# Performance work log

Measured on AMD Instinct MI355X. Metric: run time of the kernel, lower is better.

## Reference

```python
import jax, jax.numpy as jnp
import numpy as np

B, S, D, H = 4, 2048, 1024, 16
HD = D // H


def setup_inputs() -> dict:
    key = jax.random.key(0)
    k1, k2, k3 = jax.random.split(key, 3)
    x = jax.random.normal(k1, (B, S, D), dtype=jnp.float32)
    # xavier-ish scaling for stable softmax
    W_attn = jax.random.normal(k2, (3 * D, D), dtype=jnp.float32) * (1.0 / np.sqrt(2 * D))
    b_attn = jnp.zeros((3 * D,), dtype=jnp.float32)
    W_out = jax.random.normal(k3, (D, D), dtype=jnp.float32) * (1.0 / np.sqrt(D))
    b_out = jnp.zeros((D,), dtype=jnp.float32)
    return {"x": x, "W_attn": W_attn, "b_attn": b_attn, "W_out": W_out, "b_out": b_out}


def reference(x, W_attn, b_attn, W_out, b_out):
    bs, seq, d = x.shape
    # fused QKV projection (torch Linear: y = x @ W.T + b)
    kqv = jnp.einsum("bsd,ed->bse", x, W_attn) + b_attn
    # NOTE: source splits as k, q, v (k first)
    k, q, v = jnp.split(kqv, 3, axis=2)
    # [b, s, h, hd] -> [b, h, s, hd]
    k = k.reshape(bs, seq, H, HD).transpose(0, 2, 1, 3)
    q = q.reshape(bs, seq, H, HD).transpose(0, 2, 1, 3)
    v = v.reshape(bs, seq, H, HD).transpose(0, 2, 1, 3)
    scale = 1.0 / np.sqrt(HD)
    scores = jnp.einsum("bhqd,bhkd->bhqk", q, k) * scale
    attn = jax.nn.softmax(scores, axis=-1)
    y = jnp.einsum("bhqk,bhkd->bhqd", attn, v)
    y = y.transpose(0, 2, 1, 3).reshape(bs, seq, d)
    out = jnp.einsum("bsd,ed->bse", y, W_out) + b_out
    return out
```

## Files before the change

### kernel.cpp

```cpp
#include <hip/hip_runtime.h>

typedef unsigned short u16;
typedef unsigned int u32;
typedef __attribute__((ext_vector_type(2))) u32 u32x2;
typedef __attribute__((ext_vector_type(4))) u32 u32x4;
typedef __attribute__((ext_vector_type(8))) short bf16x8;
typedef __attribute__((ext_vector_type(4))) float f32x4;

__device__ __forceinline__ u16 f2bf(float f) {
  u32 b = __float_as_uint(f);
  b += 0x7fffu + ((b >> 16) & 1u);
  return (u16)(b >> 16);
}

__device__ __forceinline__ u32 pk2bf(float a, float b) {
#if __has_builtin(__builtin_amdgcn_cvt_pk_bf16_f32)
  return __builtin_bit_cast(u32, __builtin_amdgcn_cvt_pk_bf16_f32(a, b));
#else
  return (u32)f2bf(a) | ((u32)f2bf(b) << 16);
#endif
}

__device__ __forceinline__ float fexp2(float x) {
#if __has_builtin(__builtin_amdgcn_exp2f)
  return __builtin_amdgcn_exp2f(x);
#else
  return exp2f(x);
#endif
}

__device__ __forceinline__ void gload_lds16(const u16* g, u16* l) {
  __builtin_amdgcn_global_load_lds((const __attribute__((address_space(1))) void*)g,
                                   (__attribute__((address_space(3))) void*)l, 16, 0, 0);
}

__global__ __launch_bounds__(256) void cvt_f32_bf16(const float* __restrict__ in,
                                                    u16* __restrict__ out) {
  long i = ((long)blockIdx.x * 256 + threadIdx.x) * 8;
  u32 u[8];
#pragma unroll
  for (int j = 0; j < 8; j++) {
    u32 b = __float_as_uint(in[i + j]);
    u[j] = (b + 0x7fffu + ((b >> 16) & 1u)) >> 16;
  }
  u32x4 o;
  o[0] = u[0] | (u[1] << 16);
  o[1] = u[2] | (u[3] << 16);
  o[2] = u[4] | (u[5] << 16);
  o[3] = u[6] | (u[7] << 16);
  *(u32x4*)(out + i) = o;
}

__device__ __forceinline__ void gemm_core_128(const u16* __restrict__ A,
                                              const u16* __restrict__ B, int K,
                                              int m0, int n0, u16* As, u16* Bs,
                                              f32x4 acc[4][4]) {
  int t = threadIdx.x;
  int lane = t & 63, w = t >> 6;
  int quad = lane >> 4, l16 = lane & 15;
  int wm = (w >> 1) * 64, wn = (w & 1) * 64;
  int lr = lane >> 3, lc = lane & 7;
  int cg = lc ^ lr;
  int swz = l16 & 7;
  for (int k0 = 0; k0 < K; k0 += 64) {
#pragma unroll
    for (int i = 0; i < 4; i++) {
      int r0 = i * 32 + w * 8;
      gload_lds16(&A[(long)(m0 + r0 + lr) * K + k0 + cg * 8], &As[r0 * 64]);
      gload_lds16(&B[(long)(n0 + r0 + lr) * K + k0 + cg * 8], &Bs[r0 * 64]);
    }
    __syncthreads();
#pragma unroll
    for (int ks = 0; ks < 2; ks++) {
      bf16x8 a[4], b[4];
#pragma unroll
      for (int tm = 0; tm < 4; tm++)
        a[tm] = *(const bf16x8*)&As[(wm + tm * 16 + l16) * 64 + ((ks * 4 + quad) ^ swz) * 8];
#pragma unroll
      for (int tn = 0; tn < 4; tn++)
        b[tn] = *(const bf16x8*)&Bs[(wn + tn * 16 + l16) * 64 + ((ks * 4 + quad) ^ swz) * 8];
#pragma unroll
      for (int tm = 0; tm < 4; tm++)
#pragma unroll
        for (int tn = 0; tn < 4; tn++)
          acc[tm][tn] = __builtin_amdgcn_mfma_f32_16x16x32_bf16(a[tm], b[tn],
                                                                acc[tm][tn], 0, 0, 0);
    }
    __syncthreads();
  }
}

#define QSCALE 0.1803368801f
__global__ __launch_bounds__(256) void gemm_qkv(const u16* __restrict__ A,
                                                const u16* __restrict__ B,
                                                const float* __restrict__ bias,
                                                u16* __restrict__ Kg,
                                                u16* __restrict__ Qg,
                                                u16* __restrict__ Vg) {
  __shared__ __align__(16) u16 As[128 * 64];
  __shared__ __align__(16) u16 Bs[128 * 64];
  const int K = 1024;
  int m0 = blockIdx.y * 128, n0 = blockIdx.x * 128;
  f32x4 acc[4][4];
#pragma unroll
  for (int i = 0; i < 4; i++)
#pragma unroll
    for (int j = 0; j < 4; j++) acc[i][j] = (f32x4)0.0f;
  gemm_core_128(A, B, K, m0, n0, As, Bs, acc);

  int t = threadIdx.x, lane = t & 63, w = t >> 6;
  int quad = lane >> 4, l16 = lane & 15;
  int wm = (w >> 1) * 64, wn = (w & 1) * 64;
#pragma unroll
  for (int tn = 0; tn < 4; tn++) {
    int n = n0 + wn + tn * 16 + l16;
    float bv = bias[n];
    int which = n >> 10;
    int h = (n >> 6) & 15, d = n & 63;
#pragma unroll
    for (int tm = 0; tm < 4; tm++) {
      int m = m0 + wm + tm * 16 + quad * 4;
      int b = m >> 11, s = m & 2047;
      long bh = (long)b * 16 + h;
      if (which == 2) {
        u32x2 pk;
        pk[0] = pk2bf(acc[tm][tn][0] + bv, acc[tm][tn][1] + bv);
        pk[1] = pk2bf(acc[tm][tn][2] + bv, acc[tm][tn][3] + bv);
        *(u32x2*)&Vg[(bh * 64 + d) * 2048 + s] = pk;
      } else {
#pragma unroll
        for (int r = 0; r < 4; r++) {
          float v = acc[tm][tn][r] + bv;
          if (which == 0)
            Kg[(bh * 2048 + s + r) * 64 + d] = f2bf(v);
          else
            Qg[(bh * 2048 + s + r) * 64 + d] = f2bf(v * QSCALE);
        }
      }
    }
  }
}

__global__ __launch_bounds__(256) void gemm_out(const u16* __restrict__ A,
                                                const u16* __restrict__ B,
                                                const float* __restrict__ bias,
                                                float* __restrict__ out) {
  __shared__ __align__(16) u16 As[128 * 64];
  __shared__ __align__(16) u16 Bs[128 * 64];
  const int K = 1024, N = 1024;
  int m0 = blockIdx.y * 128, n0 = blockIdx.x * 128;
  f32x4 acc[4][4];
#pragma unroll
  for (int i = 0; i < 4; i++)
#pragma unroll
    for (int j = 0; j < 4; j++) acc[i][j] = (f32x4)0.0f;
  gemm_core_128(A, B, K, m0, n0, As, Bs, acc);

  int t = threadIdx.x, lane = t & 63, w = t >> 6;
  int quad = lane >> 4, l16 = lane & 15;
  int wm = (w >> 1) * 64, wn = (w & 1) * 64;
#pragma unroll
  for (int tn = 0; tn < 4; tn++) {
    int n = n0 + wn + tn * 16 + l16;
    float bv = bias[n];
#pragma unroll
    for (int tm = 0; tm < 4; tm++) {
#pragma unroll
      for (int r = 0; r < 4; r++) {
        int m = m0 + wm + tm * 16 + quad * 4 + r;
        out[(long)m * N + n] = acc[tm][tn][r] + bv;
      }
    }
  }
}

__global__ __launch_bounds__(256, 4) void attn_kernel(const u16* __restrict__ Qg,
                                                      const u16* __restrict__ Kg,
                                                      const u16* __restrict__ Vg,
                                                      u16* __restrict__ Y) {
  __shared__ __align__(16) u16 Ks[64 * 64];
  __shared__ __align__(16) u16 Vs[64 * 64];
  __shared__ __align__(16) u16 Ps[4 * 32 * 64];
  int t = threadIdx.x, lane = t & 63, w = t >> 6;
  int quad = lane >> 4, l16 = lane & 15;
  int bh = blockIdx.y;
  int q0 = blockIdx.x * 128 + w * 32;
  u16* Pw = Ps + w * 32 * 64;
  int lr = lane >> 3, lc = lane & 7, cg = lc ^ lr;
  int swz = l16 & 7;

  bf16x8 qf[2][2];
#pragma unroll
  for (int tq = 0; tq < 2; tq++) {
    const u16* qp = Qg + ((long)bh * 2048 + q0 + tq * 16 + l16) * 64;
    qf[tq][0] = *(const bf16x8*)(qp + quad * 8);
    qf[tq][1] = *(const bf16x8*)(qp + 32 + quad * 8);
  }

  float lsum[2] = {0.0f, 0.0f};
  f32x4 acc[4][2];
#pragma unroll
  for (int tn = 0; tn < 4; tn++)
#pragma unroll
    for (int tq = 0; tq < 2; tq++) acc[tn][tq] = (f32x4)0.0f;

  for (int kv0 = 0; kv0 < 2048; kv0 += 64) {
#pragma unroll
    for (int j = 0; j < 2; j++) {
      int r0 = j * 32 + w * 8;
      gload_lds16(&Kg[((long)bh * 2048 + kv0 + r0 + lr) * 64 + cg * 8], &Ks[r0 * 64]);
      gload_lds16(&Vg[((long)bh * 64 + r0 + lr) * 2048 + kv0 + cg * 8], &Vs[r0 * 64]);
    }
    __syncthreads();

    bf16x8 kf[4][2];
#pragma unroll
    for (int tn = 0; tn < 4; tn++)
#pragma unroll
      for (int ks = 0; ks < 2; ks++)
        kf[tn][ks] = *(const bf16x8*)&Ks[(tn * 16 + l16) * 64 + ((ks * 4 + quad) ^ swz) * 8];

#pragma unroll
    for (int tq = 0; tq < 2; tq++) {
      f32x4 s[4];
#pragma unroll
      for (int tn = 0; tn < 4; tn++) s[tn] = (f32x4)0.0f;
#pragma unroll
      for (int ks = 0; ks < 2; ks++)
#pragma unroll
        for (int tn = 0; tn < 4; tn++)
          s[tn] = __builtin_amdgcn_mfma_f32_16x16x32_bf16(kf[tn][ks], qf[tq][ks],
                                                          s[tn], 0, 0, 0);
      int qrow = tq * 16 + l16;
#pragma unroll
      for (int tn = 0; tn < 4; tn++) {
        float e0 = fexp2(s[tn][0]);
        float e1 = fexp2(s[tn][1]);
        float e2 = fexp2(s[tn][2]);
        float e3 = fexp2(s[tn][3]);
        lsum[tq] += (e0 + e1) + (e2 + e3);
        u32x2 pk;
        pk[0] = pk2bf(e0, e1);
        pk[1] = pk2bf(e2, e3);
        int c2 = ((tn * 2 + (quad >> 1)) ^ swz) * 2 + (quad & 1);
        *(u32x2*)&Pw[qrow * 64 + c2 * 4] = pk;
      }
    }

#pragma unroll
    for (int ks = 0; ks < 2; ks++) {
      bf16x8 vf[4];
#pragma unroll
      for (int tn = 0; tn < 4; tn++)
        vf[tn] = *(const bf16x8*)&Vs[(tn * 16 + l16) * 64 + ((ks * 4 + quad) ^ swz) * 8];
#pragma unroll
      for (int tq = 0; tq < 2; tq++) {
        bf16x8 pf = *(const bf16x8*)&Pw[(tq * 16 + l16) * 64 + ((ks * 4 + quad) ^ swz) * 8];
#pragma unroll
        for (int tn = 0; tn < 4; tn++)
          acc[tn][tq] = __builtin_amdgcn_mfma_f32_16x16x32_bf16(vf[tn], pf,
                                                                acc[tn][tq], 0, 0, 0);
      }
    }
    __syncthreads();
  }

#pragma unroll
  for (int tq = 0; tq < 2; tq++) {
    lsum[tq] += __shfl_xor(lsum[tq], 16, 64);
    lsum[tq] += __shfl_xor(lsum[tq], 32, 64);
  }

  int b = bh >> 4, h = bh & 15;
#pragma unroll
  for (int tq = 0; tq < 2; tq++) {
    float inv = 1.0f / lsum[tq];
    long row = (long)b * 2048 + q0 + tq * 16 + l16;
#pragma unroll
    for (int tn = 0; tn < 4; tn++) {
      u32x2 pk;
      pk[0] = pk2bf(acc[tn][tq][0] * inv, acc[tn][tq][1] * inv);
      pk[1] = pk2bf(acc[tn][tq][2] * inv, acc[tn][tq][3] * inv);
      *(u32x2*)&Y[row * 1024 + h * 64 + tn * 16 + quad * 4] = pk;
    }
  }
}

extern "C" void kernel_launch(void* const* d_in, const int* in_sizes, int n_in,
                              void* d_out, int out_size, void* d_ws, size_t ws_size,
                              hipStream_t stream) {
  const float* x = (const float*)d_in[0];
  const float* W_attn = (const float*)d_in[1];
  const float* b_attn = (const float*)d_in[2];
  const float* W_out = (const float*)d_in[3];
  const float* b_out = (const float*)d_in[4];
  float* out = (float*)d_out;

  char* ws = (char*)d_ws;
  u16* xb = (u16*)ws;
  u16* Wab = (u16*)(ws + 16777216);
  u16* Wob = (u16*)(ws + 16777216 + 6291456);
  u16* Kg = (u16*)(ws + 25165824);
  u16* Qg = Kg + 8388608;
  u16* Vg = Qg + 8388608;
  u16* Yb = xb;

  cvt_f32_bf16<<<4096, 256, 0, stream>>>(x, xb);
  cvt_f32_bf16<<<1536, 256, 0, stream>>>(W_attn, Wab);
  cvt_f32_bf16<<<512, 256, 0, stream>>>(W_out, Wob);

  gemm_qkv<<<dim3(24, 64), 256, 0, stream>>>(xb, Wab, b_attn, Kg, Qg, Vg);
  attn_kernel<<<dim3(16, 64), 256, 0, stream>>>(Qg, Kg, Vg, Yb);
  gemm_out<<<dim3(8, 64), 256, 0, stream>>>(Yb, Wob, b_out, out);
}
```

Measured before the change: 292.2 us.

## Double-buffer K/V tiles and keep P in registers for PV MFMA

The attention kernel now double-buffers the K and V LDS tiles, so the next tile's global-to-LDS load is issued while the current tile is being computed. The probability tile no longer round-trips through shared memory. The exponentiated scores stay in registers and feed 16x16x16 bf16 MFMAs directly, with V fragments read in the matching layout. This removes the P store/load traffic and one barrier's worth of LDS usage. The cost is twice as many PV MFMA instructions, each with half the K depth, and the double-buffered prefetch has only one barrier per iteration, which could risk an LDS race.

Result: no change. 291.6 us (-0.2%).

```diff
diff --git a/kernel.cpp b/kernel.cpp
--- a/kernel.cpp
+++ b/kernel.cpp
@@ -5,6 +5,7 @@
 typedef __attribute__((ext_vector_type(2))) u32 u32x2;
 typedef __attribute__((ext_vector_type(4))) u32 u32x4;
 typedef __attribute__((ext_vector_type(8))) short bf16x8;
+typedef __attribute__((ext_vector_type(4))) short bf16x4;
 typedef __attribute__((ext_vector_type(4))) float f32x4;
 
 __device__ __forceinline__ u16 f2bf(float f) {
@@ -21,11 +22,31 @@
 #endif
 }
 
+__device__ __forceinline__ bf16x4 mk_bf16x4(u32 lo, u32 hi) {
+  u32x2 t;
+  t[0] = lo;
+  t[1] = hi;
+  return __builtin_bit_cast(bf16x4, t);
+}
+
 __device__ __forceinline__ float fexp2(float x) {
 #if __has_builtin(__builtin_amdgcn_exp2f)
   return __builtin_amdgcn_exp2f(x);
 #else
   return exp2f(x);
+#endif
+}
+
+__device__ __forceinline__ f32x4 mfma16x16x16(bf16x4 a, bf16x4 b, f32x4 c) {
+#if __has_builtin(__builtin_amdgcn_mfma_f32_16x16x16bf16_1k)
+  return __builtin_amdgcn_mfma_f32_16x16x16bf16_1k(a, b, c, 0, 0, 0);
+#elif __has_builtin(__builtin_amdgcn_mfma_f32_16x16x16_bf16)
+  return __builtin_amdgcn_mfma_f32_16x16x16_bf16(a, b, c, 0, 0, 0);
+#else
+  asm volatile("v_mfma_f32_16x16x16_bf16 %0, %1, %2, %0\n\ts_nop 7\n\ts_nop 7"
+               : "+v"(c)
+               : "v"(a), "v"(b));
+  return c;
 #endif
 }
 
@@ -178,14 +199,12 @@
                                                       const u16* __restrict__ Kg,
                                                       const u16* __restrict__ Vg,
                                                       u16* __restrict__ Y) {
-  __shared__ __align__(16) u16 Ks[64 * 64];
-  __shared__ __align__(16) u16 Vs[64 * 64];
-  __shared__ __align__(16) u16 Ps[4 * 32 * 64];
+  __shared__ __align__(16) u16 Ks[2][64 * 64];
+  __shared__ __align__(16) u16 Vs[2][64 * 64];
   int t = threadIdx.x, lane = t & 63, w = t >> 6;
   int quad = lane >> 4, l16 = lane & 15;
   int bh = blockIdx.y;
   int q0 = blockIdx.x * 128 + w * 32;
-  u16* Pw = Ps + w * 32 * 64;
   int lr = lane >> 3, lc = lane & 7, cg = lc ^ lr;
   int swz = l16 & 7;
 
@@ -200,26 +219,43 @@
   float lsum[2] = {0.0f, 0.0f};
   f32x4 acc[4][2];
 #pragma unroll
-  for (int tn = 0; tn < 4; tn++)
-#pragma unroll
-    for (int tq = 0; tq < 2; tq++) acc[tn][tq] = (f32x4)0.0f;
-
-  for (int kv0 = 0; kv0 < 2048; kv0 += 64) {
-#pragma unroll
-    for (int j = 0; j < 2; j++) {
-      int r0 = j * 32 + w * 8;
-      gload_lds16(&Kg[((long)bh * 2048 + kv0 + r0 + lr) * 64 + cg * 8], &Ks[r0 * 64]);
-      gload_lds16(&Vg[((long)bh * 64 + r0 + lr) * 2048 + kv0 + cg * 8], &Vs[r0 * 64]);
-    }
-    __syncthreads();
+  for (int dt = 0; dt < 4; dt++)
+#pragma unroll
+    for (int tq = 0; tq < 2; tq++) acc[dt][tq] = (f32x4)0.0f;
+
+  const u16* Kbase = Kg + ((long)bh * 2048 + lr) * 64 + cg * 8;
+  const u16* Vbase = Vg + ((long)bh * 64 + lr) * 2048 + cg * 8;
+
+#pragma unroll
+  for (int j = 0; j < 2; j++) {
+    int r0 = j * 32 + w * 8;
+    gload_lds16(Kbase + (long)r0 * 64, &Ks[0][r0 * 64]);
+    gload_lds16(Vbase + (long)r0 * 2048, &Vs[0][r0 * 64]);
+  }
+  __syncthreads();
+
+  int cur = 0;
+  for (int kv0 = 0; kv0 < 2048; kv0 += 64, cur ^= 1) {
+    if (kv0 + 64 < 2048) {
+      int kn = kv0 + 64;
+#pragma unroll
+      for (int j = 0; j < 2; j++) {
+        int r0 = j * 32 + w * 8;
+        gload_lds16(Kbase + (long)(kn + r0) * 64, &Ks[cur ^ 1][r0 * 64]);
+        gload_lds16(Vbase + (long)r0 * 2048 + kn, &Vs[cur ^ 1][r0 * 64]);
+      }
+    }
+    const u16* Kc = Ks[cur];
+    const u16* Vc = Vs[cur];
 
     bf16x8 kf[4][2];
 #pragma unroll
     for (int tn = 0; tn < 4; tn++)
 #pragma unroll
       for (int ks = 0; ks < 2; ks++)
-        kf[tn][ks] = *(const bf16x8*)&Ks[(tn * 16 + l16) * 64 + ((ks * 4 + quad) ^ swz) * 8];
-
+        kf[tn][ks] = *(const bf16x8*)&Kc[(tn * 16 + l16) * 64 + ((ks * 4 + quad) ^ swz) * 8];
+
+    bf16x4 pf[2][4];
 #pragma unroll
     for (int tq = 0; tq < 2; tq++) {
       f32x4 s[4];
@@ -231,7 +267,6 @@
         for (int tn = 0; tn < 4; tn++)
           s[tn] = __builtin_amdgcn_mfma_f32_16x16x32_bf16(kf[tn][ks], qf[tq][ks],
                                                           s[tn], 0, 0, 0);
-      int qrow = tq * 16 + l16;
 #pragma unroll
       for (int tn = 0; tn < 4; tn++) {
         float e0 = fexp2(s[tn][0]);
@@ -239,28 +274,22 @@
         float e2 = fexp2(s[tn][2]);
         float e3 = fexp2(s[tn][3]);
         lsum[tq] += (e0 + e1) + (e2 + e3);
-        u32x2 pk;
-        pk[0] = pk2bf(e0, e1);
-        pk[1] = pk2bf(e2, e3);
-        int c2 = ((tn * 2 + (quad >> 1)) ^ swz) * 2 + (quad & 1);
-        *(u32x2*)&Pw[qrow * 64 + c2 * 4] = pk;
+        pf[tq][tn] = mk_bf16x4(pk2bf(e0, e1), pk2bf(e2, e3));
       }
     }
 
 #pragma unroll
-    for (int ks = 0; ks < 2; ks++) {
-      bf16x8 vf[4];
-#pragma unroll
-      for (int tn = 0; tn < 4; tn++)
-        vf[tn] = *(const bf16x8*)&Vs[(tn * 16 + l16) * 64 + ((ks * 4 + quad) ^ swz) * 8];
-#pragma unroll
-      for (int tq = 0; tq < 2; tq++) {
-        bf16x8 pf = *(const bf16x8*)&Pw[(tq * 16 + l16) * 64 + ((ks * 4 + quad) ^ swz) * 8];
-#pragma unroll
-        for (int tn = 0; tn < 4; tn++)
-          acc[tn][tq] = __builtin_amdgcn_mfma_f32_16x16x32_bf16(vf[tn], pf,
-                                                                acc[tn][tq], 0, 0, 0);
-      }
+    for (int tn = 0; tn < 4; tn++) {
+      bf16x4 vf[4];
+#pragma unroll
+      for (int dt = 0; dt < 4; dt++)
+        vf[dt] = *(const bf16x4*)&Vc[(dt * 16 + l16) * 64 +
+                                     ((tn * 2 + (quad >> 1)) ^ swz) * 8 + (quad & 1) * 4];
+#pragma unroll
+      for (int tq = 0; tq < 2; tq++)
+#pragma unroll
+        for (int dt = 0; dt < 4; dt++)
+          acc[dt][tq] = mfma16x16x16(vf[dt], pf[tq][tn], acc[dt][tq]);
     }
     __syncthreads();
   }
@@ -277,11 +306,11 @@
     float inv = 1.0f / lsum[tq];
     long row = (long)b * 2048 + q0 + tq * 16 + l16;
 #pragma unroll
-    for (int tn = 0; tn < 4; tn++) {
+    for (int dt = 0; dt < 4; dt++) {
       u32x2 pk;
-      pk[0] = pk2bf(acc[tn][tq][0] * inv, acc[tn][tq][1] * inv);
-      pk[1] = pk2bf(acc[tn][tq][2] * inv, acc[tn][tq][3] * inv);
-      *(u32x2*)&Y[row * 1024 + h * 64 + tn * 16 + quad * 4] = pk;
+      pk[0] = pk2bf(acc[dt][tq][0] * inv, acc[dt][tq][1] * inv);
+      pk[1] = pk2bf(acc[dt][tq][2] * inv, acc[dt][tq][3] * inv);
+      *(u32x2*)&Y[row * 1024 + h * 64 + dt * 16 + quad * 4] = pk;
     }
   }
 }
```
